# Performance work log

Measured on AMD Instinct MI355X. Metric: run time of the kernel, lower is better.

Reference implementation:

```python
import jax, jax.numpy as jnp
import numpy as np

D, H, KVH, HD, FF = 768, 12, 4, 64, 2048
N_REP = H // KVH
EPS = 1e-6


def rmsnorm(x, w):
    # Faithful to source: norm = ||x|| * n^{-1/2}; eps added to norm (not inside sqrt)
    norm = jnp.sqrt(jnp.sum(x * x, axis=-1, keepdims=True)) * (x.shape[-1] ** -0.5)
    return w * x / (norm + EPS)


def rope_tables(seq_len, head_dim, base=10000.0):
    inv_freq = 1.0 / (base ** (np.arange(0, head_dim, 2, dtype=np.float32) / head_dim))
    t = np.arange(seq_len, dtype=np.float32)
    freqs = np.einsum('i,j->ij', t, inv_freq)  # [S, HD/2]
    emb = np.concatenate([freqs, freqs], axis=-1)  # [S, HD]
    return jnp.asarray(np.cos(emb)), jnp.asarray(np.sin(emb))


def rotate_half(x):
    h = x.shape[-1] // 2
    return jnp.concatenate([-x[..., h:], x[..., :h]], axis=-1)


def setup_inputs() -> dict:
    key = jax.random.key(0)
    ks = jax.random.split(key, 9)
    s = 0.02
    return {
        'x': jax.random.normal(ks[0], (2, 2048, D), jnp.float32),
        'Wq': jax.random.normal(ks[1], (H * HD, D), jnp.float32) * s,
        'Wk': jax.random.normal(ks[2], (KVH * HD, D), jnp.float32) * s,
        'Wv': jax.random.normal(ks[3], (KVH * HD, D), jnp.float32) * s,
        'Wo': jax.random.normal(ks[4], (D, H * HD), jnp.float32) * s,
        'Wgate': jax.random.normal(ks[5], (FF, D), jnp.float32) * s,
        'Wup': jax.random.normal(ks[6], (FF, D), jnp.float32) * s,
        'Wdown': jax.random.normal(ks[7], (D, FF), jnp.float32) * s,
        'g1': jnp.ones((D,), jnp.float32),
        'g2': jnp.ones((D,), jnp.float32),
    }


def reference(x, Wq, Wk, Wv, Wo, Wgate, Wup, Wdown, g1, g2):
    B, S, _ = x.shape
    # ---- attention sublayer (pre-norm) ----
    xn = rmsnorm(x, g1)
    q = (xn @ Wq.T).reshape(B, S, H, HD).transpose(0, 2, 1, 3)      # [B,H,S,HD]
    k = (xn @ Wk.T).reshape(B, S, KVH, HD).transpose(0, 2, 1, 3)    # [B,KVH,S,HD]
    v = (xn @ Wv.T).reshape(B, S, KVH, HD).transpose(0, 2, 1, 3)
    cos, sin = rope_tables(S, HD)                                   # [S,HD]
    q = q * cos + rotate_half(q) * sin
    k = k * cos + rotate_half(k) * sin
    # repeat kv heads to match q heads
    k = jnp.repeat(k, N_REP, axis=1)                                # [B,H,S,HD]
    v = jnp.repeat(v, N_REP, axis=1)
    scores = jnp.einsum('bhqd,bhkd->bhqk', q, k) / jnp.sqrt(jnp.float32(HD))
    causal = jnp.tril(jnp.ones((S, S), bool))
    scores = jnp.where(causal, scores, jnp.finfo(scores.dtype).min)
    attn = jax.nn.softmax(scores, axis=-1)
    out = jnp.einsum('bhqk,bhkd->bhqd', attn, v)                    # [B,H,S,HD]
    out = out.transpose(0, 2, 1, 3).reshape(B, S, H * HD) @ Wo.T
    x = x + out
    # ---- SwiGLU FFN sublayer (pre-norm) ----
    xn2 = rmsnorm(x, g2)
    ff = (jax.nn.silu(xn2 @ Wgate.T) * (xn2 @ Wup.T)) @ Wdown.T
    return x + ff
```

## Files before the change

### kernel.cpp

```cpp
#include <hip/hip_runtime.h>
#include <hip/hip_bf16.h>
#include <math.h>

typedef __bf16 bf16;
typedef __attribute__((ext_vector_type(8))) __bf16 bf16x8;
typedef __attribute__((ext_vector_type(4))) __bf16 bf16x4;
typedef __attribute__((ext_vector_type(4))) float f32x4;

#define MFMA16(a,b,c) __builtin_amdgcn_mfma_f32_16x16x32_bf16(a,b,c,0,0,0)

#define BATCH 2
#define SEQ   2048
#define DMODEL 768
#define NH    12
#define NKV   4
#define NREP  3
#define HD    64
#define FFDIM 2048
#define ROWS  (BATCH*SEQ)

#define QSCALE 0.18033688011112042f
#define LOG2E  1.4426950408889634f

#define WB(N) asm volatile("s_waitcnt vmcnt(" #N ")\n\ts_barrier" ::: "memory")
#define BAR() asm volatile("s_barrier" ::: "memory")

__device__ __forceinline__ void gl2lds16(const bf16* g, bf16* l) {
  __builtin_amdgcn_global_load_lds(
      (const __attribute__((address_space(1))) void*)g,
      (__attribute__((address_space(3))) void*)l, 16, 0, 0);
}

struct Cvt7 { const float* s[7]; bf16* d[7]; int n[7]; float* tab; };
__global__ __launch_bounds__(256) void cvt_all_kernel(Cvt7 c) {
  int seg = blockIdx.y;
  if (seg == 7) {
    int id = blockIdx.x * 256 + threadIdx.x;
    int j = id >> 11, s = id & 2047;
    float inv = expf(-(float)j * (9.210340371976184f / 32.0f));
    float ang = (float)s * inv;
    c.tab[id] = cosf(ang);
    c.tab[65536 + id] = sinf(ang);
    return;
  }
  const float* __restrict__ src = c.s[seg];
  bf16* __restrict__ dst = c.d[seg];
  int n = c.n[seg];
  int stride = gridDim.x * 256;
  if (seg == 4 || seg == 5) {
    int up = (seg == 5) ? 32 : 0;
    for (int i = blockIdx.x * 256 + threadIdx.x; i < n; i += stride) {
      int rg = i / 768, cc = i - rg * 768;
      int drow = ((rg >> 5) << 6) + (rg & 31) + up;
      dst[(size_t)drow * 768 + cc] = (bf16)src[i];
    }
    return;
  }
  for (int i = blockIdx.x * 256 + threadIdx.x; i < n; i += stride)
    dst[i] = (bf16)src[i];
}

__global__ __launch_bounds__(192) void rmsnorm_kernel(const float* __restrict__ x,
    const float* __restrict__ g, bf16* __restrict__ out) {
  int row = blockIdx.x;
  const float* xr = x + (size_t)row * DMODEL;
  int t = threadIdx.x;
  f32x4 v = *(const f32x4*)(xr + t * 4);
  float ss = v[0] * v[0] + v[1] * v[1] + v[2] * v[2] + v[3] * v[3];
  #pragma unroll
  for (int off = 32; off; off >>= 1) ss += __shfl_xor(ss, off, 64);
  __shared__ float red[3];
  if ((t & 63) == 0) red[t >> 6] = ss;
  __syncthreads();
  float total = red[0] + red[1] + red[2];
  float norm = sqrtf(total) * 0.03608439182435161f;
  float sc = 1.0f / (norm + 1e-6f);
  f32x4 gv = *(const f32x4*)(g + t * 4);
  bf16x4 o;
  #pragma unroll
  for (int i = 0; i < 4; ++i) o[i] = (bf16)(gv[i] * v[i] * sc);
  *(bf16x4*)(out + (size_t)row * DMODEL + t * 4) = o;
}

__global__ __launch_bounds__(512, 6) void gemm_out_kernel(const bf16* __restrict__ A,
    const bf16* __restrict__ B, float* __restrict__ C, const float* __restrict__ R,
    int N, int K) {
  __shared__ __align__(16) bf16 At[2][3][64 * 32];
  __shared__ __align__(16) bf16 Bt[2][3][64 * 32];
  int t = threadIdx.x;
  int g = t >> 8;
  int tt = t & 255;
  int lane = t & 63;
  int w = (t >> 6) & 3;
  int l15 = lane & 15, lq = lane >> 4;
  int wrow = (w >> 1) * 32, wcol = (w & 1) * 32;

  int flat = blockIdx.y * 12 + blockIdx.x;
  int f2 = (flat & 7) * 96 + (flat >> 3);
  int col0 = (f2 % 12) * 64, row0 = (f2 / 12) * 64;

  const int KH = K >> 1;
  const int NS = KH / 32;
  const bf16* Ag = A + (size_t)(row0 + (tt >> 2)) * K + g * KH + (tt & 3) * 8;
  const bf16* Bg = B + (size_t)(col0 + (tt >> 2)) * K + g * KH + (tt & 3) * 8;

  #pragma unroll
  for (int s = 0; s < 2; ++s) {
    gl2lds16(Ag + s * 32, At[g][s] + tt * 8);
    gl2lds16(Bg + s * 32, Bt[g][s] + tt * 8);
  }

  f32x4 zero = {0.f, 0.f, 0.f, 0.f};
  f32x4 acc[2][2];
  #pragma unroll
  for (int m = 0; m < 2; ++m)
    #pragma unroll
    for (int n = 0; n < 2; ++n) acc[m][n] = zero;

  #define OG_COMPUTE(slot) do {                                              \
    const bf16* at = At[g][slot]; const bf16* bt = Bt[g][slot];              \
    bf16x8 af[2], bb[2];                                                     \
    _Pragma("unroll")                                                        \
    for (int m = 0; m < 2; ++m)                                              \
      af[m] = *(const bf16x8*)(at + (wrow + m * 16 + l15) * 32 + lq * 8);    \
    _Pragma("unroll")                                                        \
    for (int n = 0; n < 2; ++n)                                              \
      bb[n] = *(const bf16x8*)(bt + (wcol + n * 16 + l15) * 32 + lq * 8);    \
    _Pragma("unroll")                                                        \
    for (int m = 0; m < 2; ++m)                                              \
      _Pragma("unroll")                                                      \
      for (int n = 0; n < 2; ++n)                                            \
        acc[m][n] = MFMA16(af[m], bb[n], acc[m][n]);                         \
  } while (0)

  int slot = 0;
  for (int k = 0; k < NS - 1; ++k) {
    WB(2);
    if (k + 2 < NS) {
      int ks = (k + 2) * 32;
      int ws = slot + 2; if (ws >= 3) ws -= 3;
      gl2lds16(Ag + ks, At[g][ws] + tt * 8);
      gl2lds16(Bg + ks, Bt[g][ws] + tt * 8);
    }
    OG_COMPUTE(slot);
    slot = (slot == 2) ? 0 : slot + 1;
  }
  WB(0);
  OG_COMPUTE(slot);
  #undef OG_COMPUTE

  __syncthreads();
  float* Cl = (float*)&At[0][0][0];
  if (g == 1) {
    #pragma unroll
    for (int m = 0; m < 2; ++m)
      #pragma unroll
      for (int n = 0; n < 2; ++n)
        #pragma unroll
        for (int r = 0; r < 4; ++r)
          Cl[(wrow + m * 16 + lq * 4 + r) * 64 + wcol + n * 16 + l15] = acc[m][n][r];
  }
  __syncthreads();
  if (g == 0) {
    #pragma unroll
    for (int m = 0; m < 2; ++m)
      #pragma unroll
      for (int n = 0; n < 2; ++n)
        #pragma unroll
        for (int r = 0; r < 4; ++r) {
          int row = wrow + m * 16 + lq * 4 + r;
          int col = wcol + n * 16 + l15;
          size_t idx = (size_t)(row0 + row) * N + col0 + col;
          C[idx] = acc[m][n][r] + Cl[row * 64 + col] + R[idx];
        }
  }
}

__global__ __launch_bounds__(256) void gemm_qkv_kernel(const bf16* __restrict__ A,
    const bf16* __restrict__ Wcat, const float* __restrict__ tab,
    bf16* __restrict__ Qh, bf16* __restrict__ Kh, bf16* __restrict__ Vt) {
  __shared__ __align__(16) bf16 At[4][64 * 32];
  __shared__ __align__(16) bf16 Bt[4][128 * 32];
  const int K = DMODEL;
  int t = threadIdx.x, lane = t & 63, wave = t >> 6;
  int l15 = lane & 15, lq = lane >> 4;
  int wrow = (wave >> 1) * 32, wcol = (wave & 1) * 64;
  int row0 = blockIdx.y * 64, col0 = blockIdx.x * 128;
  const bf16* Ag  = A + (size_t)(row0 + (t >> 2)) * K + (t & 3) * 8;
  const bf16* Bg0 = Wcat + (size_t)(col0 + (t >> 2)) * K + (t & 3) * 8;
  const bf16* Bg1 = Bg0 + (size_t)64 * K;
  const int NS = K / 32;

  #pragma unroll
  for (int s = 0; s < 3; ++s) {
    int ks = s * 32;
    gl2lds16(Ag + ks,  At[s] + t * 8);
    gl2lds16(Bg0 + ks, Bt[s] + t * 8);
    gl2lds16(Bg1 + ks, Bt[s] + 2048 + t * 8);
  }

  f32x4 zero = {0.f, 0.f, 0.f, 0.f};
  f32x4 acc[2][4];
  #pragma unroll
  for (int m = 0; m < 2; ++m)
    #pragma unroll
    for (int n = 0; n < 4; ++n) acc[m][n] = zero;

  #define QK_COMPUTE(slot) do {                                              \
    const bf16* at = At[slot]; const bf16* bt = Bt[slot];                    \
    bf16x8 af[2], bfr[4];                                                    \
    _Pragma("unroll")                                                        \
    for (int m = 0; m < 2; ++m)                                              \
      af[m] = *(const bf16x8*)(at + (wrow + m * 16 + l15) * 32 + lq * 8);    \
    _Pragma("unroll")                                                        \
    for (int n = 0; n < 4; ++n)                                              \
      bfr[n] = *(const bf16x8*)(bt + (wcol + n * 16 + l15) * 32 + lq * 8);   \
    _Pragma("unroll")                                                        \
    for (int m = 0; m < 2; ++m)                                              \
      _Pragma("unroll")                                                      \
      for (int n = 0; n < 4; ++n)                                            \
        acc[m][n] = MFMA16(af[m], bfr[n], acc[m][n]);                        \
  } while (0)

  for (int k = 0; k < NS - 2; ++k) {
    WB(6);
    if (k + 3 < NS) {
      int ks = (k + 3) * 32;
      int ws = (k + 3) & 3;
      gl2lds16(Ag + ks,  At[ws] + t * 8);
      gl2lds16(Bg0 + ks, Bt[ws] + t * 8);
      gl2lds16(Bg1 + ks, Bt[ws] + 2048 + t * 8);
    }
    QK_COMPUTE(k & 3);
  }
  WB(3);
  QK_COMPUTE((NS - 2) & 3);
  WB(0);
  QK_COMPUTE((NS - 1) & 3);
  #undef QK_COMPUTE

  int b = row0 >> 11;
  int s0 = (row0 & 2047) + wrow + lq * 4;
  int colw = col0 + wcol;
  if (colw < 768) {
    int h = colw >> 6;
    f32x4 cv[2][2], sv[2][2];
    #pragma unroll
    for (int m = 0; m < 2; ++m)
      #pragma unroll
      for (int jh = 0; jh < 2; ++jh) {
        const float* cp = tab + (jh * 16 + l15) * 2048 + s0 + m * 16;
        cv[m][jh] = *(const f32x4*)cp;
        sv[m][jh] = *(const f32x4*)(cp + 65536);
      }
    #pragma unroll
    for (int m = 0; m < 2; ++m)
      #pragma unroll
      for (int n = 0; n < 4; ++n) {
        float sgn = (n < 2) ? -1.f : 1.f;
        #pragma unroll
        for (int r = 0; r < 4; ++r) {
          float c = cv[m][n & 1][r], si = sv[m][n & 1][r];
          float rp = (acc[m][n][r] * c + sgn * acc[m][n ^ 2][r] * si) * QSCALE;
          Qh[((size_t)(b * NH + h) * SEQ + s0 + m * 16 + r) * 64 + n * 16 + l15] = (bf16)rp;
        }
      }
  } else if (colw < 1024) {
    int kh = (colw - 768) >> 6;
    f32x4 cv[2][2], sv[2][2];
    #pragma unroll
    for (int m = 0; m < 2; ++m)
      #pragma unroll
      for (int jh = 0; jh < 2; ++jh) {
        const float* cp = tab + (jh * 16 + l15) * 2048 + s0 + m * 16;
        cv[m][jh] = *(const f32x4*)cp;
        sv[m][jh] = *(const f32x4*)(cp + 65536);
      }
    #pragma unroll
    for (int m = 0; m < 2; ++m)
      #pragma unroll
      for (int n = 0; n < 4; ++n) {
        float sgn = (n < 2) ? -1.f : 1.f;
        #pragma unroll
        for (int r = 0; r < 4; ++r) {
          float c = cv[m][n & 1][r], si = sv[m][n & 1][r];
          float rp = acc[m][n][r] * c + sgn * acc[m][n ^ 2][r] * si;
          Kh[((size_t)(b * NKV + kh) * SEQ + s0 + m * 16 + r) * 64 + n * 16 + l15] = (bf16)rp;
        }
      }
  } else {
    int vh = (colw - 1024) >> 6;
    #pragma unroll
    for (int m = 0; m < 2; ++m)
      #pragma unroll
      for (int n = 0; n < 4; ++n) {
        bf16x4 pv;
        #pragma unroll
        for (int r = 0; r < 4; ++r) pv[r] = (bf16)acc[m][n][r];
        *(bf16x4*)(Vt + ((size_t)(b * NKV + vh) * 64 + n * 16 + l15) * SEQ + s0 + m * 16) = pv;
      }
  }
}

__global__ __launch_bounds__(512, 2) void gemm_gu_kernel(const bf16* __restrict__ A,
    const bf16* __restrict__ W, bf16* __restrict__ H) {
  __shared__ __align__(16) bf16 Als[2 * 2 * 128 * 64];
  __shared__ __align__(16) bf16 Bls[2 * 2 * 128 * 64];
  const int NT = 12;
  int t = threadIdx.x, lane = t & 63, wave = t >> 6;
  int l15 = lane & 15, lq = lane >> 4;
  int lfrag = l15 * 32 + lq * 8;
  int wm = wave >> 2, wn = wave & 3;

  int flat = blockIdx.y * 16 + blockIdx.x;
  int f2 = (flat & 7) * 32 + (flat >> 3);
  int colb = f2 & 15, rowb = f2 >> 4;
  int row0 = rowb * 256, col0w = colb * 256;

  #define STAGE(G, orow, L, j, h) do {                                       \
    bf16* lb = (L) + ((j) & 1) * 16384 + (h) * 8192 + t * 8;                 \
    const bf16* gb = (G) + (size_t)((orow) + (h) * 128 + ((t >> 7) << 4)     \
                   + ((t >> 2) & 15)) * 768 + (j) * 64                       \
                   + ((t >> 6) & 1) * 32 + (t & 3) * 8;                      \
    gl2lds16(gb, lb);                                                        \
    gl2lds16(gb + (size_t)64 * 768, lb + 4096);                              \
  } while (0)

  STAGE(W, col0w, Bls, 0, 0);  STAGE(W, col0w, Bls, 0, 1);
  STAGE(A, row0,  Als, 0, 0);  STAGE(A, row0,  Als, 0, 1);
  STAGE(W, col0w, Bls, 1, 0);  STAGE(W, col0w, Bls, 1, 1);

  f32x4 zero = {0.f, 0.f, 0.f, 0.f};
  f32x4 acc[8][4];
  #pragma unroll
  for (int m = 0; m < 8; ++m)
    #pragma unroll
    for (int n = 0; n < 4; ++n) acc[m][n] = zero;

  WB(4);

  for (int j = 0; j < NT; ++j) {
    const bf16* aB = Als + (j & 1) * 16384 + wm * 8192 + lfrag;
    const bf16* bB = Bls + (j & 1) * 16384 + (wn >> 1) * 8192 + (wn & 1) * 4096 + lfrag;
    bf16x8 afr[4][2], bfr[4][2];

    #pragma unroll
    for (int m = 0; m < 4; ++m)
      #pragma unroll
      for (int kk = 0; kk < 2; ++kk)
        afr[m][kk] = *(const bf16x8*)(aB + m * 1024 + kk * 512);
    #pragma unroll
    for (int n = 0; n < 2; ++n)
      #pragma unroll
      for (int kk = 0; kk < 2; ++kk)
        bfr[n][kk] = *(const bf16x8*)(bB + n * 1024 + kk * 512);
    if (j + 1 < NT) STAGE(A, row0, Als, j + 1, 0);
    BAR();
    __builtin_amdgcn_s_setprio(1);
    #pragma unroll
    for (int m = 0; m < 4; ++m)
      #pragma unroll
      for (int n = 0; n < 2; ++n) {
        acc[m][n] = MFMA16(afr[m][0], bfr[n][0], acc[m][n]);
        acc[m][n] = MFMA16(afr[m][1], bfr[n][1], acc[m][n]);
      }
    __builtin_amdgcn_s_setprio(0);
    BAR();

    #pragma unroll
    for (int n = 2; n < 4; ++n)
      #pragma unroll
      for (int kk = 0; kk < 2; ++kk)
        bfr[n][kk] = *(const bf16x8*)(bB + n * 1024 + kk * 512);
    if (j + 1 < NT) STAGE(A, row0, Als, j + 1, 1);
    BAR();
    __builtin_amdgcn_s_setprio(1);
    #pragma unroll
    for (int m = 0; m < 4; ++m)
      #pragma unroll
      for (int n = 2; n < 4; ++n) {
        acc[m][n] = MFMA16(afr[m][0], bfr[n][0], acc[m][n]);
        acc[m][n] = MFMA16(afr[m][1], bfr[n][1], acc[m][n]);
      }
    __builtin_amdgcn_s_setprio(0);
    BAR();

    #pragma unroll
    for (int m = 0; m < 4; ++m)
      #pragma unroll
      for (int kk = 0; kk < 2; ++kk)
        afr[m][kk] = *(const bf16x8*)(aB + (m + 4) * 1024 + kk * 512);
    if (j + 2 < NT) STAGE(W, col0w, Bls, j + 2, 0);
    BAR();
    __builtin_amdgcn_s_setprio(1);
    #pragma unroll
    for (int m = 0; m < 4; ++m)
      #pragma unroll
      for (int n = 0; n < 2; ++n) {
        acc[m + 4][n] = MFMA16(afr[m][0], bfr[n][0], acc[m + 4][n]);
        acc[m + 4][n] = MFMA16(afr[m][1], bfr[n][1], acc[m + 4][n]);
      }
    __builtin_amdgcn_s_setprio(0);
    BAR();

    if (j + 2 < NT) STAGE(W, col0w, Bls, j + 2, 1);
    BAR();
    __builtin_amdgcn_s_setprio(1);
    #pragma unroll
    for (int m = 0; m < 4; ++m)
      #pragma unroll
      for (int n = 2; n < 4; ++n) {
        acc[m + 4][n] = MFMA16(afr[m][0], bfr[n][0], acc[m + 4][n]);
        acc[m + 4][n] = MFMA16(afr[m][1], bfr[n][1], acc[m + 4][n]);
      }
    __builtin_amdgcn_s_setprio(0);
    if (j < NT - 2)       WB(4);
    else if (j == NT - 2) WB(0);
  }
  #undef STAGE

  int hc0 = colb * 128 + wn * 32;
  #pragma unroll
  for (int m = 0; m < 8; ++m)
    #pragma unroll
    for (int n = 0; n < 2; ++n)
      #pragma unroll
      for (int r = 0; r < 4; ++r) {
        int row = row0 + wm * 128 + m * 16 + lq * 4 + r;
        int col = hc0 + n * 16 + l15;
        float g = acc[m][n][r], u = acc[m][n + 2][r];
        float sg = g / (1.f + __builtin_amdgcn_exp2f(-g * LOG2E));
        H[(size_t)row * FFDIM + col] = (bf16)(sg * u);
      }
}

__global__ __launch_bounds__(256) void attn_kernel(const bf16* __restrict__ Qh,
    const bf16* __restrict__ Kh, const bf16* __restrict__ Vt, bf16* __restrict__ out) {
  __shared__ __align__(16) bf16 Kl0[2][64 * 32];
  __shared__ __align__(16) bf16 Kl1[2][64 * 32];
  __shared__ __align__(16) bf16 Vl0[2][64 * 32];
  __shared__ __align__(16) bf16 Vl1[2][64 * 32];
  __shared__ __align__(16) bf16 P[4][16 * 72];

  int idx = blockIdx.x;
  int qt = 31 - (idx / 24);
  int bh = idx % 24;
  int q0blk = qt * 64;
  int b = bh / NH, h = bh % NH;
  int kvh = h / NREP;
  int t = threadIdx.x;
  int lane = t & 63, wave = t >> 6;
  int l15 = lane & 15, lq = lane >> 4;
  int qw = q0blk + wave * 16;
  const bf16* Qb = Qh + (size_t)(b * NH + h) * SEQ * 64;
  const bf16* Kb = Kh + (size_t)(b * NKV + kvh) * SEQ * 64;
  const bf16* Vb = Vt + (size_t)(b * NKV + kvh) * 64 * SEQ;

  bf16x8 bq0 = *(const bf16x8*)(Qb + (size_t)(qw + l15) * 64 + lq * 8);
  bf16x8 bq1 = *(const bf16x8*)(Qb + (size_t)(qw + l15) * 64 + 32 + lq * 8);

  int srow = (t >> 6) * 16 + ((t >> 2) & 15);
  int scol = (t & 3) * 8;
  const bf16* Kg = Kb + (size_t)srow * 64 + scol;
  const bf16* Vg = Vb + (size_t)srow * SEQ + scol;
  bf16* Pw = P[wave];
  int Pwq = l15 * 72, lq8 = lq * 8, lq4 = lq * 4;
  int lfrag = l15 * 32 + lq8;
  const int NS = qt + 1;

  #pragma unroll
  for (int s = 0; s < 2; ++s) {
    int ks = (s < NS ? s : NS - 1) * 64;
    gl2lds16(Kg + (size_t)ks * 64,      Kl0[s] + t * 8);
    gl2lds16(Kg + (size_t)ks * 64 + 32, Kl1[s] + t * 8);
    gl2lds16(Vg + ks,                   Vl0[s] + t * 8);
    gl2lds16(Vg + ks + 32,              Vl1[s] + t * 8);
  }

  f32x4 zero = {0.f, 0.f, 0.f, 0.f};
  f32x4 o[4];
  o[0] = zero; o[1] = zero; o[2] = zero; o[3] = zero;
  float l_r = 0.f;

  #define ATTN_STEP(kk, slot) do {                                           \
    int k0 = (kk) * 64;                                                      \
    const bf16* kl0 = Kl0[slot]; const bf16* kl1 = Kl1[slot];                \
    const bf16* vl0 = Vl0[slot]; const bf16* vl1 = Vl1[slot];                \
    f32x4 s[4];                                                              \
    _Pragma("unroll")                                                        \
    for (int c = 0; c < 4; ++c) {                                            \
      bf16x8 ak0 = *(const bf16x8*)(kl0 + c * 512 + lfrag);                  \
      bf16x8 ak1 = *(const bf16x8*)(kl1 + c * 512 + lfrag);                  \
      s[c] = zero;                                                           \
      s[c] = MFMA16(ak0, bq0, s[c]);                                         \
      s[c] = MFMA16(ak1, bq1, s[c]);                                         \
    }                                                                        \
    if (k0 + 63 > qw) {                                                      \
      int qmk = qw + l15 - k0 - lq4;                                         \
      _Pragma("unroll")                                                      \
      for (int c = 0; c < 4; ++c)                                            \
        _Pragma("unroll")                                                    \
        for (int r = 0; r < 4; ++r)                                          \
          if (c * 16 + r > qmk) s[c][r] = -INFINITY;                         \
    }                                                                        \
    _Pragma("unroll")                                                        \
    for (int c = 0; c < 4; ++c) {                                            \
      bf16x4 pe;                                                             \
      _Pragma("unroll")                                                      \
      for (int r = 0; r < 4; ++r) {                                          \
        float e = __builtin_amdgcn_exp2f(s[c][r]);                           \
        l_r += e;                                                            \
        pe[r] = (bf16)e;                                                     \
      }                                                                      \
      *(bf16x4*)(Pw + Pwq + c * 16 + lq4) = pe;                              \
    }                                                                        \
    bf16x8 bp0 = *(const bf16x8*)(Pw + Pwq + lq8);                           \
    bf16x8 bp1 = *(const bf16x8*)(Pw + Pwq + 32 + lq8);                      \
    _Pragma("unroll")                                                        \
    for (int n = 0; n < 4; ++n) {                                            \
      bf16x8 av0 = *(const bf16x8*)(vl0 + n * 512 + lfrag);                  \
      bf16x8 av1 = *(const bf16x8*)(vl1 + n * 512 + lfrag);                  \
      o[n] = MFMA16(av0, bp0, o[n]);                                         \
      o[n] = MFMA16(av1, bp1, o[n]);                                         \
    }                                                                        \
  } while (0)

  for (int k = 0; k < NS - 1; ++k) {
    WB(4);
    ATTN_STEP(k, k & 1);
    BAR();
    if (k <= NS - 3) {
      int ks = (k + 2) * 64;
      gl2lds16(Kg + (size_t)ks * 64,      Kl0[k & 1] + t * 8);
      gl2lds16(Kg + (size_t)ks * 64 + 32, Kl1[k & 1] + t * 8);
      gl2lds16(Vg + ks,                   Vl0[k & 1] + t * 8);
      gl2lds16(Vg + ks + 32,              Vl1[k & 1] + t * 8);
    }
  }
  {
    WB(0);
    ATTN_STEP(NS - 1, (NS - 1) & 1);
  }
  #undef ATTN_STEP

  float lt = l_r;
  lt += __shfl_xor(lt, 16, 64);
  lt += __shfl_xor(lt, 32, 64);
  float inv = 1.f / lt;
  int q = qw + l15;
  bf16* orow = out + (size_t)(b * SEQ + q) * DMODEL + h * 64;
  #pragma unroll
  for (int n = 0; n < 4; ++n) {
    bf16x4 po;
    #pragma unroll
    for (int r = 0; r < 4; ++r) po[r] = (bf16)(o[n][r] * inv);
    *(bf16x4*)(orow + n * 16 + lq4) = po;
  }
}

extern "C" void kernel_launch(void* const* d_in, const int* in_sizes, int n_in,
                              void* d_out, int out_size, void* d_ws, size_t ws_size,
                              hipStream_t stream) {
  const float* x     = (const float*)d_in[0];
  const float* Wq    = (const float*)d_in[1];
  const float* Wk    = (const float*)d_in[2];
  const float* Wv    = (const float*)d_in[3];
  const float* Wo    = (const float*)d_in[4];
  const float* Wgate = (const float*)d_in[5];
  const float* Wup   = (const float*)d_in[6];
  const float* Wdown = (const float*)d_in[7];
  const float* g1    = (const float*)d_in[8];
  const float* g2    = (const float*)d_in[9];
  float* out = (float*)d_out;

  char* ws = (char*)d_ws;
  size_t off = 0;
  auto alloc = [&](size_t bytes) { size_t o = off; off += (bytes + 255) & ~(size_t)255; return o; };
  size_t o_tab  = alloc((size_t)2 * 32 * 2048 * 4);
  size_t o_x1   = alloc((size_t)4096 * 768 * 4);
  size_t o_xn   = alloc((size_t)4096 * 768 * 2);
  size_t o_Qh   = alloc((size_t)2 * 12 * 2048 * 64 * 2);
  size_t o_Kh   = alloc((size_t)2 * 4 * 2048 * 64 * 2);
  size_t o_Vt   = alloc((size_t)2 * 4 * 64 * 2048 * 2);
  size_t o_ao   = alloc((size_t)4096 * 768 * 2);
  size_t o_H    = alloc((size_t)4096 * 2048 * 2);
  size_t o_Wcat = alloc((size_t)1280 * 768 * 2);
  size_t o_Wo   = alloc((size_t)768 * 768 * 2);
  size_t o_Wgu  = alloc((size_t)4096 * 768 * 2);
  size_t o_Wdn  = alloc((size_t)768 * 2048 * 2);
  if (ws_size < off) return;

  float* tab  = (float*)(ws + o_tab);
  float* fx1  = (float*)(ws + o_x1);
  bf16* bxn   = (bf16*)(ws + o_xn);
  bf16* bQh   = (bf16*)(ws + o_Qh);
  bf16* bKh   = (bf16*)(ws + o_Kh);
  bf16* bVt   = (bf16*)(ws + o_Vt);
  bf16* bao   = (bf16*)(ws + o_ao);
  bf16* bH    = (bf16*)(ws + o_H);
  bf16* bWcat = (bf16*)(ws + o_Wcat);
  bf16* bWo   = (bf16*)(ws + o_Wo);
  bf16* bWgu  = (bf16*)(ws + o_Wgu);
  bf16* bWdn  = (bf16*)(ws + o_Wdn);

  Cvt7 c;
  c.s[0] = Wq;    c.d[0] = bWcat;              c.n[0] = 768 * 768;
  c.s[1] = Wk;    c.d[1] = bWcat + 768 * 768;  c.n[1] = 256 * 768;
  c.s[2] = Wv;    c.d[2] = bWcat + 1024 * 768; c.n[2] = 256 * 768;
  c.s[3] = Wo;    c.d[3] = bWo;                c.n[3] = 768 * 768;
  c.s[4] = Wgate; c.d[4] = bWgu;               c.n[4] = 2048 * 768;
  c.s[5] = Wup;   c.d[5] = bWgu;               c.n[5] = 2048 * 768;
  c.s[6] = Wdown; c.d[6] = bWdn;               c.n[6] = 768 * 2048;
  c.tab = tab;
  cvt_all_kernel<<<dim3(256, 8), 256, 0, stream>>>(c);

  rmsnorm_kernel<<<4096, 192, 0, stream>>>(x, g1, bxn);
  gemm_qkv_kernel<<<dim3(10, 64), 256, 0, stream>>>(bxn, bWcat, tab, bQh, bKh, bVt);
  attn_kernel<<<dim3(768), 256, 0, stream>>>(bQh, bKh, bVt, bao);
  gemm_out_kernel<<<dim3(12, 64), 512, 0, stream>>>(bao, bWo, fx1, x, 768, 768);

  rmsnorm_kernel<<<4096, 192, 0, stream>>>(fx1, g2, bxn);
  gemm_gu_kernel<<<dim3(16, 16), 512, 0, stream>>>(bxn, bWgu, bH);
  gemm_out_kernel<<<dim3(12, 64), 512, 0, stream>>>(bH, bWdn, out, fx1, 768, 2048);
}
```

Baseline: 238.5 us.

## Split long causal attention tiles across two blocks and combine partials

Query tiles 16-31, which have the longest causal key ranges, are split into two key-range halves processed by separate blocks, scheduled through a lookup table that interleaves long and short jobs. Each split half writes unnormalized fp32 partial outputs and row sums to workspace, and a new combine kernel adds them and normalizes into the bf16 output. The goal is better load balance and less tail imbalance across CUs. The cost is extra fp32 traffic and one extra kernel launch. The combine relies on the softmax having no running max, so adding the raw exponential sums is valid.

```diff
diff --git a/kernel.cpp b/kernel.cpp
--- a/kernel.cpp
+++ b/kernel.cpp
@@ -434,8 +434,21 @@
       }
 }
 
+__device__ const unsigned char JT[48][3] = {
+  {31,0,16},{31,16,32},{30,0,16},{15,0,16},
+  {30,16,31},{29,0,15},{29,15,30},{28,0,15},{14,0,15},
+  {28,15,29},{27,0,14},{27,14,28},{26,0,14},{13,0,14},
+  {26,14,27},{25,0,13},{25,13,26},{24,0,13},{12,0,13},
+  {24,13,25},{23,0,12},{23,12,24},{22,0,12},{11,0,12},
+  {22,12,23},{21,0,11},{21,11,22},{20,0,11},{10,0,11},
+  {20,11,21},{19,0,10},{19,10,20},{18,0,10},{9,0,10},
+  {18,10,19},{17,0,9},{17,9,18},{16,0,9},{8,0,9},
+  {16,9,17},{7,0,8},
+  {6,0,7},{5,0,6},{4,0,5},{3,0,4},{2,0,3},{1,0,2},{0,0,1}};
+
 __global__ __launch_bounds__(256) void attn_kernel(const bf16* __restrict__ Qh,
-    const bf16* __restrict__ Kh, const bf16* __restrict__ Vt, bf16* __restrict__ out) {
+    const bf16* __restrict__ Kh, const bf16* __restrict__ Vt, bf16* __restrict__ out,
+    float* __restrict__ opart, float* __restrict__ lpart) {
   __shared__ __align__(16) bf16 Kl0[2][64 * 32];
   __shared__ __align__(16) bf16 Kl1[2][64 * 32];
   __shared__ __align__(16) bf16 Vl0[2][64 * 32];
@@ -443,8 +456,11 @@
   __shared__ __align__(16) bf16 P[4][16 * 72];
 
   int idx = blockIdx.x;
-  int qt = 31 - (idx / 24);
-  int bh = idx % 24;
+  int job = idx / 24, bh = idx % 24;
+  int qt   = JT[job][0];
+  int kbeg = JT[job][1];
+  int kend = JT[job][2];
+  const int NSL = kend - kbeg;
   int q0blk = qt * 64;
   int b = bh / NH, h = bh % NH;
   int kvh = h / NREP;
@@ -466,11 +482,10 @@
   bf16* Pw = P[wave];
   int Pwq = l15 * 72, lq8 = lq * 8, lq4 = lq * 4;
   int lfrag = l15 * 32 + lq8;
-  const int NS = qt + 1;
 
   #pragma unroll
   for (int s = 0; s < 2; ++s) {
-    int ks = (s < NS ? s : NS - 1) * 64;
+    int ks = (kbeg + (s < NSL ? s : NSL - 1)) * 64;
     gl2lds16(Kg + (size_t)ks * 64,      Kl0[s] + t * 8);
     gl2lds16(Kg + (size_t)ks * 64 + 32, Kl1[s] + t * 8);
     gl2lds16(Vg + ks,                   Vl0[s] + t * 8);
@@ -525,12 +540,12 @@
     }                                                                        \
   } while (0)
 
-  for (int k = 0; k < NS - 1; ++k) {
+  for (int k = 0; k < NSL - 1; ++k) {
     WB(4);
-    ATTN_STEP(k, k & 1);
-    BAR();
-    if (k <= NS - 3) {
-      int ks = (k + 2) * 64;
+    ATTN_STEP(kbeg + k, k & 1);
+    BAR();
+    if (k <= NSL - 3) {
+      int ks = (kbeg + k + 2) * 64;
       gl2lds16(Kg + (size_t)ks * 64,      Kl0[k & 1] + t * 8);
       gl2lds16(Kg + (size_t)ks * 64 + 32, Kl1[k & 1] + t * 8);
       gl2lds16(Vg + ks,                   Vl0[k & 1] + t * 8);
@@ -539,22 +554,54 @@
   }
   {
     WB(0);
-    ATTN_STEP(NS - 1, (NS - 1) & 1);
+    ATTN_STEP(kbeg + NSL - 1, (NSL - 1) & 1);
   }
   #undef ATTN_STEP
 
   float lt = l_r;
   lt += __shfl_xor(lt, 16, 64);
   lt += __shfl_xor(lt, 32, 64);
-  float inv = 1.f / lt;
-  int q = qw + l15;
-  bf16* orow = out + (size_t)(b * SEQ + q) * DMODEL + h * 64;
-  #pragma unroll
-  for (int n = 0; n < 4; ++n) {
+  if (qt >= 16) {
+    int slot = ((31 - qt) * 24 + bh) * 2 + (kbeg != 0);
+    float* ob = opart + (size_t)slot * 4096 + (wave * 16 + l15) * 64;
+    #pragma unroll
+    for (int n = 0; n < 4; ++n) *(f32x4*)(ob + n * 16 + lq4) = o[n];
+    if (lq == 0) lpart[slot * 64 + wave * 16 + l15] = lt;
+  } else {
+    float inv = 1.f / lt;
+    int q = qw + l15;
+    bf16* orow = out + (size_t)(b * SEQ + q) * DMODEL + h * 64;
+    #pragma unroll
+    for (int n = 0; n < 4; ++n) {
+      bf16x4 po;
+      #pragma unroll
+      for (int r = 0; r < 4; ++r) po[r] = (bf16)(o[n][r] * inv);
+      *(bf16x4*)(orow + n * 16 + lq4) = po;
+    }
+  }
+}
+
+__global__ __launch_bounds__(256) void attn_combine_kernel(
+    const float* __restrict__ opart, const float* __restrict__ lpart,
+    bf16* __restrict__ out) {
+  int tile = blockIdx.x;
+  int rank = tile / 24, bh = tile % 24;
+  int qt = 31 - rank;
+  int b = bh / NH, h = bh % NH;
+  int t = threadIdx.x;
+  const float* o0 = opart + (size_t)tile * 2 * 4096;
+  const float* o1 = o0 + 4096;
+  const float* l0 = lpart + tile * 2 * 64;
+  const float* l1 = l0 + 64;
+  for (int i = t; i < 1024; i += 256) {
+    int row = i >> 4, c4 = (i & 15) * 4;
+    f32x4 a = *(const f32x4*)(o0 + row * 64 + c4);
+    f32x4 bb = *(const f32x4*)(o1 + row * 64 + c4);
+    float inv = 1.f / (l0[row] + l1[row]);
     bf16x4 po;
     #pragma unroll
-    for (int r = 0; r < 4; ++r) po[r] = (bf16)(o[n][r] * inv);
-    *(bf16x4*)(orow + n * 16 + lq4) = po;
+    for (int r = 0; r < 4; ++r) po[r] = (bf16)((a[r] + bb[r]) * inv);
+    *(bf16x4*)(out + (size_t)(b * SEQ + qt * 64 + row) * DMODEL + h * 64 + c4) = po;
   }
 }
 
@@ -588,6 +635,8 @@
   size_t o_Wo   = alloc((size_t)768 * 768 * 2);
   size_t o_Wgu  = alloc((size_t)4096 * 768 * 2);
   size_t o_Wdn  = alloc((size_t)768 * 2048 * 2);
+  size_t o_op   = alloc((size_t)384 * 2 * 4096 * 4);
+  size_t o_lp   = alloc((size_t)384 * 2 * 64 * 4);
   if (ws_size < off) return;
 
   float* tab  = (float*)(ws + o_tab);
@@ -602,6 +651,8 @@
   bf16* bWo   = (bf16*)(ws + o_Wo);
   bf16* bWgu  = (bf16*)(ws + o_Wgu);
   bf16* bWdn  = (bf16*)(ws + o_Wdn);
+  float* opart = (float*)(ws + o_op);
+  float* lpart = (float*)(ws + o_lp);
 
   Cvt7 c;
   c.s[0] = Wq;    c.d[0] = bWcat;              c.n[0] = 768 * 768;
@@ -616,7 +667,8 @@
 
   rmsnorm_kernel<<<4096, 192, 0, stream>>>(x, g1, bxn);
   gemm_qkv_kernel<<<dim3(10, 64), 256, 0, stream>>>(bxn, bWcat, tab, bQh, bKh, bVt);
-  attn_kernel<<<dim3(768), 256, 0, stream>>>(bQh, bKh, bVt, bao);
+  attn_kernel<<<dim3(1152), 256, 0, stream>>>(bQh, bKh, bVt, bao, opart, lpart);
+  attn_combine_kernel<<<dim3(384), 256, 0, stream>>>(opart, lpart, bao);
   gemm_out_kernel<<<dim3(12, 64), 512, 0, stream>>>(bao, bWo, fx1, x, 768, 768);
 
   rmsnorm_kernel<<<4096, 192, 0, stream>>>(fx1, g2, bxn);
```

Result: no change. 243.0 us (+1.9%).
